# Kernel optimization log

Hardware: AMD Instinct MI355X
Metric: run time of the kernel (lower is better)

The kernel has to match this reference:

```python
import jax, jax.numpy as jnp
import numpy as np

B, T, C = 4, 2048, 1024
H = 16
HD = C // H  # 64


def setup_inputs() -> dict:
    key = jax.random.key(0)
    ks = jax.random.split(key, 5)
    x = jax.random.normal(ks[0], (B, T, C), dtype=jnp.float32)
    # torch nn.Linear weights have shape [out_features, in_features]
    s = 1.0 / np.sqrt(C)
    Wq = jax.random.uniform(ks[1], (C, C), jnp.float32, -s, s)
    Wk = jax.random.uniform(ks[2], (C, C), jnp.float32, -s, s)
    Wv = jax.random.uniform(ks[3], (C, C), jnp.float32, -s, s)
    Wo = jax.random.uniform(ks[4], (C, C), jnp.float32, -s, s)
    return {"x": x, "Wq": Wq, "Wk": Wk, "Wv": Wv, "Wo": Wo}


def _split_heads(t):
    b, s, c = t.shape
    return t.reshape(b, s, H, HD).transpose(0, 2, 1, 3)  # [B,H,T,HD]


def reference(x, Wq, Wk, Wv, Wo):
    q = _split_heads(x @ Wq.T)
    k = _split_heads(x @ Wk.T)
    v = _split_heads(x @ Wv.T)
    scale = 1.0 / np.sqrt(HD).astype(np.float32)
    scores = jnp.einsum('bhqd,bhkd->bhqk', q, k) * scale  # [B,H,T,T]
    causal = jnp.tril(jnp.ones((T, T), dtype=bool))
    scores = jnp.where(causal[None, None], scores, -jnp.inf)
    weights = jax.nn.softmax(scores, axis=-1)
    ctx = jnp.einsum('bhqk,bhkd->bhqd', weights, v)
    y = ctx.transpose(0, 2, 1, 3).reshape(x.shape[0], x.shape[1], C)
    return y @ Wo.T
```

## Files before the change

### kernel.cpp

```cpp
#include <hip/hip_runtime.h>

typedef __attribute__((ext_vector_type(8))) short short8;
typedef __attribute__((ext_vector_type(4))) float floatx4;
typedef __attribute__((ext_vector_type(16))) float floatx16;

__device__ __forceinline__ ushort f2bf(float f) {
  unsigned u = __float_as_uint(f);
  u += 0x7fffu + ((u >> 16) & 1u);
  return (ushort)(u >> 16);
}

__device__ __forceinline__ uint2 pack4(floatx4 v, float scale) {
  unsigned p0 = __float_as_uint(v[0] * scale) + 0x8000u;
  unsigned p1 = __float_as_uint(v[1] * scale) + 0x8000u;
  unsigned p2 = __float_as_uint(v[2] * scale) + 0x8000u;
  unsigned p3 = __float_as_uint(v[3] * scale) + 0x8000u;
  uint2 w;
  w.x = __builtin_amdgcn_perm(p1, p0, 0x07060302);
  w.y = __builtin_amdgcn_perm(p3, p2, 0x07060302);
  return w;
}

__device__ __forceinline__ uint2 pack4f(float a, float b, float c, float d, float scale) {
  floatx4 v;
  v[0] = a; v[1] = b; v[2] = c; v[3] = d;
  return pack4(v, scale);
}

__device__ __forceinline__ void gll16(const ushort* g, ushort* l) {
  __builtin_amdgcn_global_load_lds(
      (const __attribute__((address_space(1))) unsigned int*)(g),
      (__attribute__((address_space(3))) unsigned int*)(l), 16, 0, 0);
}

__global__ void cvt_all(const float* __restrict__ x, const float* __restrict__ a,
                        const float* __restrict__ b, const float* __restrict__ c,
                        const float* __restrict__ d, ushort* __restrict__ ox,
                        ushort* __restrict__ oa, ushort* __restrict__ ob,
                        ushort* __restrict__ oc, ushort* __restrict__ od) {
  int bid = blockIdx.x;
  const float* in;
  ushort* out;
  int lb;
  if (bid < 8192) { in = x; out = ox; lb = bid; }
  else {
    int w = (bid - 8192) >> 10;
    lb = (bid - 8192) & 1023;
    in = w == 0 ? a : (w == 1 ? b : (w == 2 ? c : d));
    out = w == 0 ? oa : (w == 1 ? ob : (w == 2 ? oc : od));
  }
  int i = (lb * 256 + threadIdx.x) * 4;
  float4 v = *(const float4*)(in + i);
  ushort4 o = make_ushort4(f2bf(v.x), f2bf(v.y), f2bf(v.z), f2bf(v.w));
  *(ushort4*)(out + i) = o;
}

__device__ __forceinline__ void stage64(const ushort* __restrict__ G, size_t gstride,
                                        int grow0, int gcol0, ushort* __restrict__ S,
                                        int wave, int lane) {
  int r8 = lane >> 3;
  int sc = ((lane & 7) ^ (r8 & 7)) * 8;
  for (int c = 0; c < 4; c++) {
    int rl = wave * 32 + c * 8;
    gll16(&G[(size_t)(grow0 + rl + r8) * gstride + gcol0 + sc], &S[rl * 64]);
  }
}

__global__ __launch_bounds__(256) void gemm_qkv(const ushort* __restrict__ A,
                                                const ushort* __restrict__ W0,
                                                const ushort* __restrict__ W1,
                                                const ushort* __restrict__ W2,
                                                ushort* __restrict__ Qb,
                                                ushort* __restrict__ Kb,
                                                ushort* __restrict__ VT) {
  __shared__ __align__(16) ushort sA[128 * 64];
  __shared__ __align__(16) ushort sB[128 * 64];
  const int K = 1024;
  int tid = threadIdx.x, wave = tid >> 6, lane = tid & 63;
  int h = lane >> 5, r5 = lane & 31, l7 = lane & 7;
  int bid = blockIdx.x;
  int mblk = bid & 63, nblk = bid >> 6;
  int m0 = mblk * 128;
  int mat = nblk >> 3;
  int n0 = (nblk & 7) * 128;
  const ushort* Bw = mat == 0 ? W0 : (mat == 1 ? W1 : W2);
  bool qkpath = (mat < 2);

  floatx16 acc[2][2];
  for (int i = 0; i < 2; i++)
    for (int t = 0; t < 2; t++) acc[i][t] = (floatx16)0.0f;
  int mrow = (wave >> 1) * 64, ncol = (wave & 1) * 64;

  const ushort* PA = qkpath ? sB : sA;
  const ushort* PB = qkpath ? sA : sB;
  int aoff = qkpath ? ncol : mrow;
  int boff = qkpath ? mrow : ncol;

  for (int k0 = 0; k0 < K; k0 += 64) {
    __syncthreads();
    stage64(A, K, m0, k0, sA, wave, lane);
    stage64(Bw, K, n0, k0, sB, wave, lane);
    __syncthreads();
    for (int ks = 0; ks < 4; ks++) {
      int cs = ((ks * 2 + h) ^ l7) * 8;
      short8 af[2], bf[2];
      for (int i = 0; i < 2; i++) af[i] = *(const short8*)&PA[(aoff + i * 32 + r5) * 64 + cs];
      for (int t = 0; t < 2; t++) bf[t] = *(const short8*)&PB[(boff + t * 32 + r5) * 64 + cs];
      for (int i = 0; i < 2; i++)
        for (int t = 0; t < 2; t++)
          acc[i][t] = __builtin_amdgcn_mfma_f32_32x32x16_bf16(af[i], bf[t], acc[i][t], 0, 0, 0);
    }
  }

  if (qkpath) {
    float qs = (mat == 0) ? 0.18033688f : 1.0f;
    ushort* dst = (mat == 0) ? Qb : Kb;
    for (int i = 0; i < 2; i++) {
      for (int t = 0; t < 2; t++) {
        for (int g = 0; g < 4; g++) {
          int n = n0 + ncol + i * 32 + 4 * h + 8 * g;
          int m = m0 + mrow + t * 32 + r5;
          int b = m >> 11, tt = m & 2047, hh = n >> 6, hd = n & 63;
          *(uint2*)&dst[((((size_t)b * 16 + hh) * 2048 + tt) << 6) + hd] =
              pack4f(acc[i][t][4 * g], acc[i][t][4 * g + 1],
                     acc[i][t][4 * g + 2], acc[i][t][4 * g + 3], qs);
        }
      }
    }
  } else {
    for (int i = 0; i < 2; i++) {
      for (int t = 0; t < 2; t++) {
        for (int g = 0; g < 4; g++) {
          int m = m0 + mrow + i * 32 + 4 * h + 8 * g;
          int n = n0 + ncol + t * 32 + r5;
          int b = m >> 11, tt = m & 2047, hh = n >> 6, hd = n & 63;
          *(uint2*)&VT[(((size_t)b * 16 + hh) * 64 + hd) * 2048 + tt] =
              pack4f(acc[i][t][4 * g], acc[i][t][4 * g + 1],
                     acc[i][t][4 * g + 2], acc[i][t][4 * g + 3], 1.0f);
        }
      }
    }
  }
}

__global__ __launch_bounds__(256) void gemm_out(const ushort* __restrict__ A,
                                                const ushort* __restrict__ W0,
                                                float* __restrict__ Fout) {
  __shared__ __align__(16) ushort sA[128 * 64];
  __shared__ __align__(16) ushort sB[128 * 64];
  const int K = 1024;
  int tid = threadIdx.x, wave = tid >> 6, lane = tid & 63;
  int h = lane >> 5, r5 = lane & 31, l7 = lane & 7;
  int bid = blockIdx.x;
  int m0 = (bid & 63) * 128;
  int n0 = (bid >> 6) * 128;

  floatx16 acc[2][2];
  for (int i = 0; i < 2; i++)
    for (int t = 0; t < 2; t++) acc[i][t] = (floatx16)0.0f;
  int mrow = (wave >> 1) * 64, ncol = (wave & 1) * 64;

  for (int k0 = 0; k0 < K; k0 += 64) {
    __syncthreads();
    stage64(A, K, m0, k0, sA, wave, lane);
    stage64(W0, K, n0, k0, sB, wave, lane);
    __syncthreads();
    for (int ks = 0; ks < 4; ks++) {
      int cs = ((ks * 2 + h) ^ l7) * 8;
      short8 af[2], bf[2];
      for (int i = 0; i < 2; i++) af[i] = *(const short8*)&sB[(ncol + i * 32 + r5) * 64 + cs];
      for (int t = 0; t < 2; t++) bf[t] = *(const short8*)&sA[(mrow + t * 32 + r5) * 64 + cs];
      for (int i = 0; i < 2; i++)
        for (int t = 0; t < 2; t++)
          acc[i][t] = __builtin_amdgcn_mfma_f32_32x32x16_bf16(af[i], bf[t], acc[i][t], 0, 0, 0);
    }
  }

  for (int i = 0; i < 2; i++) {
    for (int t = 0; t < 2; t++) {
      for (int g = 0; g < 4; g++) {
        int n = n0 + ncol + i * 32 + 4 * h + 8 * g;
        int m = m0 + mrow + t * 32 + r5;
        floatx4 v;
        v[0] = acc[i][t][4 * g];
        v[1] = acc[i][t][4 * g + 1];
        v[2] = acc[i][t][4 * g + 2];
        v[3] = acc[i][t][4 * g + 3];
        *(floatx4*)&Fout[(size_t)m * 1024 + n] = v;
      }
    }
  }
}

#define SD 76
__global__ __launch_bounds__(256) void attn(const ushort* __restrict__ Qb,
                                            const ushort* __restrict__ Kb,
                                            const ushort* __restrict__ VTb,
                                            ushort* __restrict__ ctx) {
  __shared__ __align__(16) ushort sK[64 * 64];
  __shared__ __align__(16) ushort sVT[64 * 64];
  __shared__ __align__(16) ushort sP[128 * SD];

  int tid = threadIdx.x, wave = tid >> 6, lane = tid & 63;
  int ln = lane & 15, quad = lane >> 4;
  int bid = blockIdx.x;
  int hi = bid >> 8, lo = bid & 255;
  int u = lo & 3;
  int bh = lo >> 2;
  int qb = (hi == 0) ? (15 - 2 * u)
         : (hi == 1) ? (2 * u)
         : (hi == 2) ? (14 - 2 * u)
                     : (2 * u + 1);

  const ushort* Qp = Qb + (size_t)bh * 2048 * 64 + (size_t)qb * 128 * 64;
  const ushort* Kp = Kb + (size_t)bh * 2048 * 64;
  const ushort* VTp = VTb + (size_t)bh * 64 * 2048;

  for (int i = 0; i < 4; i++) {
    int e = tid + i * 256;
    int row = e >> 3, c8 = (e & 7) * 8;
    *(uint4*)&sP[row * SD + c8] = *(const uint4*)&Qp[row * 64 + c8];
  }
  __syncthreads();
  short8 qf[2][2];
  for (int f = 0; f < 2; f++)
    for (int ks = 0; ks < 2; ks++)
      qf[f][ks] = *(const short8*)&sP[(wave * 32 + f * 16 + ln) * SD + ks * 32 + quad * 8];

  floatx4 o[2][4];
  for (int f = 0; f < 2; f++)
    for (int t = 0; t < 4; t++) o[f][t] = (floatx4)0.0f;
  float l_acc[2] = {0.0f, 0.0f};

  int kt_m = 2 * qb + (wave >> 1);
  int ktend = 2 * qb + 1;
  int r8 = lane >> 3;
  int scs = ((lane & 7) ^ (r8 & 7)) * 8;

  for (int kt = 0; kt <= ktend; kt++) {
    __syncthreads();
    for (int c = 0; c < 2; c++) {
      int rl = wave * 16 + c * 8;
      gll16(&Kp[(size_t)(kt * 64 + rl + r8) * 64 + scs], &sK[rl * 64]);
      gll16(&VTp[(size_t)(rl + r8) * 2048 + kt * 64 + scs], &sVT[rl * 64]);
    }
    __syncthreads();
    if (kt > kt_m) continue;

    floatx4 s[2][4];
    for (int f = 0; f < 2; f++)
      for (int t = 0; t < 4; t++) s[f][t] = (floatx4)0.0f;
    for (int ks = 0; ks < 2; ks++) {
      int cs = ((ks * 4 + quad) ^ (ln & 7)) * 8;
      short8 kf[4];
      for (int t = 0; t < 4; t++)
        kf[t] = *(const short8*)&sK[(t * 16 + ln) * 64 + cs];
      for (int f = 0; f < 2; f++)
        for (int t = 0; t < 4; t++)
          s[f][t] = __builtin_amdgcn_mfma_f32_16x16x32_bf16(kf[t], qf[f][ks], s[f][t], 0, 0, 0);
    }

    if (kt == kt_m) {
      for (int f = 0; f < 2; f++) {
        int qg = qb * 128 + wave * 32 + f * 16 + ln;
        for (int t = 0; t < 4; t++) {
          int kg = kt * 64 + t * 16 + quad * 4;
          for (int r2 = 0; r2 < 4; r2++)
            if (kg + r2 > qg) s[f][t][r2] = -1e30f;
        }
      }
    }

    for (int f = 0; f < 2; f++) {
      int prow = (wave * 32 + f * 16 + ln) * SD;
      for (int t = 0; t < 4; t++) {
        floatx4 p;
        for (int r2 = 0; r2 < 4; r2++) {
          p[r2] = __builtin_amdgcn_exp2f(s[f][t][r2]);
          l_acc[f] += p[r2];
        }
        *(uint2*)&sP[prow + t * 16 + quad * 4] = pack4(p, 1.0f);
      }
    }

    for (int ks = 0; ks < 2; ks++) {
      int cs = ((ks * 4 + quad) ^ (ln & 7)) * 8;
      short8 vf[4];
      for (int t = 0; t < 4; t++)
        vf[t] = *(const short8*)&sVT[(t * 16 + ln) * 64 + cs];
      for (int f = 0; f < 2; f++) {
        short8 pf = *(const short8*)&sP[(wave * 32 + f * 16 + ln) * SD + ks * 32 + quad * 8];
        for (int t = 0; t < 4; t++)
          o[f][t] = __builtin_amdgcn_mfma_f32_16x16x32_bf16(pf, vf[t], o[f][t], 0, 0, 0);
      }
    }
  }

  for (int f = 0; f < 2; f++) {
    l_acc[f] += __shfl_xor(l_acc[f], 16);
    l_acc[f] += __shfl_xor(l_acc[f], 32);
  }

  int b = bh >> 4, h = bh & 15;
  for (int f = 0; f < 2; f++) {
    for (int r2 = 0; r2 < 4; r2++) {
      float lr = __shfl(l_acc[f], quad * 4 + r2);
      float linv = 1.0f / lr;
      int qg = qb * 128 + wave * 32 + f * 16 + quad * 4 + r2;
      for (int t = 0; t < 4; t++) {
        int col = h * 64 + t * 16 + ln;
        ctx[((size_t)b * 2048 + qg) * 1024 + col] = f2bf(o[f][t][r2] * linv);
      }
    }
  }
}

extern "C" void kernel_launch(void* const* d_in, const int* in_sizes, int n_in,
                              void* d_out, int out_size, void* d_ws, size_t ws_size,
                              hipStream_t stream) {
  const float* x  = (const float*)d_in[0];
  const float* Wq = (const float*)d_in[1];
  const float* Wk = (const float*)d_in[2];
  const float* Wv = (const float*)d_in[3];
  const float* Wo = (const float*)d_in[4];
  float* out = (float*)d_out;

  char* ws = (char*)d_ws;
  const size_t MB = 1024 * 1024;
  ushort* xb   = (ushort*)(ws + 0);
  ushort* Wqb  = (ushort*)(ws + 16 * MB);
  ushort* Wkb  = (ushort*)(ws + 18 * MB);
  ushort* Wvb  = (ushort*)(ws + 20 * MB);
  ushort* Wob  = (ushort*)(ws + 22 * MB);
  ushort* Qb   = (ushort*)(ws + 24 * MB);
  ushort* Kb   = (ushort*)(ws + 40 * MB);
  ushort* Vtb  = (ushort*)(ws + 56 * MB);
  ushort* ctxb = xb;

  cvt_all<<<12288, 256, 0, stream>>>(x, Wq, Wk, Wv, Wo, xb, Wqb, Wkb, Wvb, Wob);

  gemm_qkv<<<1536, 256, 0, stream>>>(xb, Wqb, Wkb, Wvb, Qb, Kb, Vtb);
  attn<<<1024, 256, 0, stream>>>(Qb, Kb, Vtb, ctxb);
  gemm_out<<<512, 256, 0, stream>>>(ctxb, Wob, out);
}
```

Measured before the change: 243.5 us.

## Double-buffer LDS tiles in GEMM and attention kernels to overlap loads

Both GEMM kernels and the attention kernel get two LDS buffers per operand. Each loop iteration now issues the async global-to-LDS load for the next K-tile (or K/V tile) before running the MFMAs on the current one, and only one barrier per iteration remains instead of two. The aim is to hide global memory latency behind matrix compute. In exchange, the GEMM kernels double their LDS use to 64KB per block, which may lower occupancy. The overlap also depends on the compiler not inserting a full vmcnt wait before the LDS reads.

```diff
diff --git a/kernel.cpp b/kernel.cpp
--- a/kernel.cpp
+++ b/kernel.cpp
@@ -73,8 +73,8 @@
                                                 ushort* __restrict__ Qb,
                                                 ushort* __restrict__ Kb,
                                                 ushort* __restrict__ VT) {
-  __shared__ __align__(16) ushort sA[128 * 64];
-  __shared__ __align__(16) ushort sB[128 * 64];
+  __shared__ __align__(16) ushort sA[2][128 * 64];
+  __shared__ __align__(16) ushort sB[2][128 * 64];
   const int K = 1024;
   int tid = threadIdx.x, wave = tid >> 6, lane = tid & 63;
   int h = lane >> 5, r5 = lane & 31, l7 = lane & 7;
@@ -90,17 +90,21 @@
   for (int i = 0; i < 2; i++)
     for (int t = 0; t < 2; t++) acc[i][t] = (floatx16)0.0f;
   int mrow = (wave >> 1) * 64, ncol = (wave & 1) * 64;
-
-  const ushort* PA = qkpath ? sB : sA;
-  const ushort* PB = qkpath ? sA : sB;
   int aoff = qkpath ? ncol : mrow;
   int boff = qkpath ? mrow : ncol;
 
-  for (int k0 = 0; k0 < K; k0 += 64) {
+  stage64(A, K, m0, 0, sA[0], wave, lane);
+  stage64(Bw, K, n0, 0, sB[0], wave, lane);
+
+  for (int kb = 0; kb < 16; kb++) {
     __syncthreads();
-    stage64(A, K, m0, k0, sA, wave, lane);
-    stage64(Bw, K, n0, k0, sB, wave, lane);
-    __syncthreads();
+    int cur = kb & 1;
+    if (kb + 1 < 16) {
+      stage64(A, K, m0, (kb + 1) * 64, sA[cur ^ 1], wave, lane);
+      stage64(Bw, K, n0, (kb + 1) * 64, sB[cur ^ 1], wave, lane);
+    }
+    const ushort* PA = qkpath ? sB[cur] : sA[cur];
+    const ushort* PB = qkpath ? sA[cur] : sB[cur];
     for (int ks = 0; ks < 4; ks++) {
       int cs = ((ks * 2 + h) ^ l7) * 8;
       short8 af[2], bf[2];
@@ -146,8 +150,8 @@
 __global__ __launch_bounds__(256) void gemm_out(const ushort* __restrict__ A,
                                                 const ushort* __restrict__ W0,
                                                 float* __restrict__ Fout) {
-  __shared__ __align__(16) ushort sA[128 * 64];
-  __shared__ __align__(16) ushort sB[128 * 64];
+  __shared__ __align__(16) ushort sA[2][128 * 64];
+  __shared__ __align__(16) ushort sB[2][128 * 64];
   const int K = 1024;
   int tid = threadIdx.x, wave = tid >> 6, lane = tid & 63;
   int h = lane >> 5, r5 = lane & 31, l7 = lane & 7;
@@ -160,16 +164,21 @@
     for (int t = 0; t < 2; t++) acc[i][t] = (floatx16)0.0f;
   int mrow = (wave >> 1) * 64, ncol = (wave & 1) * 64;
 
-  for (int k0 = 0; k0 < K; k0 += 64) {
+  stage64(A, K, m0, 0, sA[0], wave, lane);
+  stage64(W0, K, n0, 0, sB[0], wave, lane);
+
+  for (int kb = 0; kb < 16; kb++) {
     __syncthreads();
-    stage64(A, K, m0, k0, sA, wave, lane);
-    stage64(W0, K, n0, k0, sB, wave, lane);
-    __syncthreads();
+    int cur = kb & 1;
+    if (kb + 1 < 16) {
+      stage64(A, K, m0, (kb + 1) * 64, sA[cur ^ 1], wave, lane);
+      stage64(W0, K, n0, (kb + 1) * 64, sB[cur ^ 1], wave, lane);
+    }
     for (int ks = 0; ks < 4; ks++) {
       int cs = ((ks * 2 + h) ^ l7) * 8;
       short8 af[2], bf[2];
-      for (int i = 0; i < 2; i++) af[i] = *(const short8*)&sB[(ncol + i * 32 + r5) * 64 + cs];
-      for (int t = 0; t < 2; t++) bf[t] = *(const short8*)&sA[(mrow + t * 32 + r5) * 64 + cs];
+      for (int i = 0; i < 2; i++) af[i] = *(const short8*)&sB[cur][(ncol + i * 32 + r5) * 64 + cs];
+      for (int t = 0; t < 2; t++) bf[t] = *(const short8*)&sA[cur][(mrow + t * 32 + r5) * 64 + cs];
       for (int i = 0; i < 2; i++)
         for (int t = 0; t < 2; t++)
           acc[i][t] = __builtin_amdgcn_mfma_f32_32x32x16_bf16(af[i], bf[t], acc[i][t], 0, 0, 0);
@@ -197,8 +206,8 @@
                                             const ushort* __restrict__ Kb,
                                             const ushort* __restrict__ VTb,
                                             ushort* __restrict__ ctx) {
-  __shared__ __align__(16) ushort sK[64 * 64];
-  __shared__ __align__(16) ushort sVT[64 * 64];
+  __shared__ __align__(16) ushort sK[2][64 * 64];
+  __shared__ __align__(16) ushort sVT[2][64 * 64];
   __shared__ __align__(16) ushort sP[128 * SD];
 
   int tid = threadIdx.x, wave = tid >> 6, lane = tid & 63;
@@ -216,6 +225,15 @@
   const ushort* Kp = Kb + (size_t)bh * 2048 * 64;
   const ushort* VTp = VTb + (size_t)bh * 64 * 2048;
 
+  int r8 = lane >> 3;
+  int scs = ((lane & 7) ^ (r8 & 7)) * 8;
+
+  for (int c = 0; c < 2; c++) {
+    int rl = wave * 16 + c * 8;
+    gll16(&Kp[(size_t)(rl + r8) * 64 + scs], &sK[0][rl * 64]);
+    gll16(&VTp[(size_t)(rl + r8) * 2048 + scs], &sVT[0][rl * 64]);
+  }
+
   for (int i = 0; i < 4; i++) {
     int e = tid + i * 256;
     int row = e >> 3, c8 = (e & 7) * 8;
@@ -234,17 +252,17 @@
 
   int kt_m = 2 * qb + (wave >> 1);
   int ktend = 2 * qb + 1;
-  int r8 = lane >> 3;
-  int scs = ((lane & 7) ^ (r8 & 7)) * 8;
 
   for (int kt = 0; kt <= ktend; kt++) {
     __syncthreads();
-    for (int c = 0; c < 2; c++) {
-      int rl = wave * 16 + c * 8;
-      gll16(&Kp[(size_t)(kt * 64 + rl + r8) * 64 + scs], &sK[rl * 64]);
-      gll16(&VTp[(size_t)(rl + r8) * 2048 + kt * 64 + scs], &sVT[rl * 64]);
-    }
-    __syncthreads();
+    int cur = kt & 1;
+    if (kt + 1 <= ktend) {
+      for (int c = 0; c < 2; c++) {
+        int rl = wave * 16 + c * 8;
+        gll16(&Kp[(size_t)((kt + 1) * 64 + rl + r8) * 64 + scs], &sK[cur ^ 1][rl * 64]);
+        gll16(&VTp[(size_t)(rl + r8) * 2048 + (kt + 1) * 64 + scs], &sVT[cur ^ 1][rl * 64]);
+      }
+    }
     if (kt > kt_m) continue;
 
     floatx4 s[2][4];
@@ -254,7 +272,7 @@
       int cs = ((ks * 4 + quad) ^ (ln & 7)) * 8;
       short8 kf[4];
       for (int t = 0; t < 4; t++)
-        kf[t] = *(const short8*)&sK[(t * 16 + ln) * 64 + cs];
+        kf[t] = *(const short8*)&sK[cur][(t * 16 + ln) * 64 + cs];
       for (int f = 0; f < 2; f++)
         for (int t = 0; t < 4; t++)
           s[f][t] = __builtin_amdgcn_mfma_f32_16x16x32_bf16(kf[t], qf[f][ks], s[f][t], 0, 0, 0);
@@ -287,7 +305,7 @@
       int cs = ((ks * 4 + quad) ^ (ln & 7)) * 8;
       short8 vf[4];
       for (int t = 0; t < 4; t++)
-        vf[t] = *(const short8*)&sVT[(t * 16 + ln) * 64 + cs];
+        vf[t] = *(const short8*)&sVT[cur][(t * 16 + ln) * 64 + cs];
       for (int f = 0; f < 2; f++) {
         short8 pf = *(const short8*)&sP[(wave * 32 + f * 16 + ln) * SD + ks * 32 + quad * 8];
         for (int t = 0; t < 4; t++)
```

After: 252.9 us. 1.04x slower.
